# Kernel optimization log

Hardware: AMD Instinct MI355X
Metric: run time of the kernel (lower is better)

Reference implementation:

```python
import jax, jax.numpy as jnp
import numpy as np

N = 50000
E = 600000
IN_DIM, FEAT_DIM, HID_DIM, OUT_DIM = 256, 128, 128, 64


def _glorot(key, shape):
    fan_in, fan_out = shape[0], shape[1]
    lim = jnp.sqrt(6.0 / (fan_in + fan_out))
    return jax.random.uniform(key, shape, jnp.float32, -lim, lim)


def setup_inputs() -> dict:
    key = jax.random.key(0)
    ks = jax.random.split(key, 10)
    x = jax.random.normal(ks[0], (N, IN_DIM), jnp.float32)
    edge_index = jax.random.randint(ks[1], (2, E), 0, N, jnp.int64)
    return {
        "x": x,
        "edge_index": edge_index,
        # linear_pre: input_dim -> feature_dim
        "W_pre": _glorot(ks[2], (IN_DIM, FEAT_DIM)),
        "b_pre": jnp.zeros((FEAT_DIM,), jnp.float32),
        # conv_first (SAGEConv feature_dim -> hidden_dim): lin_l (neighbors, bias), lin_r (root, no bias)
        "Wl1": _glorot(ks[3], (FEAT_DIM, HID_DIM)),
        "bl1": jnp.zeros((HID_DIM,), jnp.float32),
        "Wr1": _glorot(ks[4], (FEAT_DIM, HID_DIM)),
        # conv_out (SAGEConv hidden_dim -> output_dim)
        "Wl2": _glorot(ks[5], (HID_DIM, OUT_DIM)),
        "bl2": jnp.zeros((OUT_DIM,), jnp.float32),
        "Wr2": _glorot(ks[6], (HID_DIM, OUT_DIM)),
    }


def _sage_conv(x, src, dst, deg_inv, Wl, bl, Wr):
    # mean aggregation of source features at destination nodes
    msgs = x[src]                                            # [E, d]
    aggr = jax.ops.segment_sum(msgs, dst, num_segments=N)    # [N, d]
    aggr = aggr * deg_inv[:, None]
    return aggr @ Wl + bl + x @ Wr


def reference(x, edge_index, W_pre, b_pre, Wl1, bl1, Wr1, Wl2, bl2, Wr2):
    src, dst = edge_index[0], edge_index[1]
    deg = jax.ops.segment_sum(jnp.ones((E,), jnp.float32), dst, num_segments=N)
    deg_inv = jnp.where(deg > 0, 1.0 / jnp.maximum(deg, 1.0), 0.0)

    h = x @ W_pre + b_pre                                    # linear_pre
    h = _sage_conv(h, src, dst, deg_inv, Wl1, bl1, Wr1)      # conv_first
    h = jax.nn.relu(h)
    # dropout: identity in eval mode
    h = _sage_conv(h, src, dst, deg_inv, Wl2, bl2, Wr2)      # conv_out
    norm = jnp.linalg.norm(h, axis=-1, keepdims=True)
    return h / jnp.maximum(norm, 1e-12)                      # F.normalize p=2
```

## Files before the change

### kernel.cpp

```cpp
#include <hip/hip_runtime.h>


#define NN   50000
#define EE   600000
#define NBLK 49
#define NRG  1563
#define GEMM_BLOCKS 512

typedef __attribute__((ext_vector_type(8))) _Float16 h8v;
typedef __attribute__((ext_vector_type(4))) _Float16 h4v;
typedef __attribute__((ext_vector_type(2))) _Float16 h2v;
typedef __attribute__((ext_vector_type(8))) short short8v;
typedef __attribute__((ext_vector_type(4))) float f32x4;

__device__ inline h8v h8zero() {
    return __builtin_bit_cast(h8v, (short8v){0,0,0,0,0,0,0,0});
}


__global__ __launch_bounds__(256) void k_count(const int* __restrict__ ei,
                                               int* __restrict__ counts) {
    int e = blockIdx.x * 256 + threadIdx.x;
    if (e < EE) atomicAdd(&counts[ei[EE + e]], 1);
}

__global__ __launch_bounds__(256) void k_scan_a(const int* __restrict__ counts,
                                                int* __restrict__ bsums) {
    int b = blockIdx.x, t = threadIdx.x;
    int idx = b * 1024 + t * 4;
    int s = 0;
#pragma unroll
    for (int j = 0; j < 4; ++j)
        if (idx + j < NN) s += counts[idx + j];
#pragma unroll
    for (int off = 32; off > 0; off >>= 1) s += __shfl_down(s, off);
    __shared__ int ls[4];
    if ((t & 63) == 0) ls[t >> 6] = s;
    __syncthreads();
    if (t == 0) bsums[b] = ls[0] + ls[1] + ls[2] + ls[3];
}

__global__ void k_scan_b(int* __restrict__ bsums) {
    int t = threadIdx.x;
    int v = (t < NBLK) ? bsums[t] : 0;
    int orig = v;
#pragma unroll
    for (int off = 1; off < 64; off <<= 1) {
        int u = __shfl_up(v, off);
        if (t >= off) v += u;
    }
    if (t < NBLK) bsums[t] = v - orig;
}

__global__ __launch_bounds__(256) void k_scan_c(const int* __restrict__ counts,
                                                const int* __restrict__ bsums,
                                                int* __restrict__ rowp) {
    int b = blockIdx.x, t = threadIdx.x;
    int lane = t & 63, wave = t >> 6;
    int idx = b * 1024 + t * 4;
    int c[4], s = 0;
#pragma unroll
    for (int j = 0; j < 4; ++j) {
        c[j] = (idx + j < NN) ? counts[idx + j] : 0;
        s += c[j];
    }
    int sv = s;
#pragma unroll
    for (int off = 1; off < 64; off <<= 1) {
        int u = __shfl_up(sv, off);
        if (lane >= off) sv += u;
    }
    __shared__ int lsum[4];
    if (lane == 63) lsum[wave] = sv;
    __syncthreads();
    int woff = 0;
    for (int wv = 0; wv < wave; ++wv) woff += lsum[wv];
    int base = bsums[b] + woff + (sv - s);
#pragma unroll
    for (int j = 0; j < 4; ++j) {
        if (idx + j < NN) { rowp[idx + j] = base; base += c[j]; }
    }
}

__global__ __launch_bounds__(256) void k_scatter(const int* __restrict__ ei,
                                                 const int* __restrict__ rowp,
                                                 int* __restrict__ cursor,
                                                 int* __restrict__ col) {
    int e = blockIdx.x * 256 + threadIdx.x;
    if (e < EE) {
        int d = ei[EE + e];
        int p = atomicAdd(&cursor[d], 1);
        col[rowp[d] + p] = ei[e];
    }
}


__global__ __launch_bounds__(256) void k_cvt(const float* __restrict__ in,
                                             _Float16* __restrict__ outp, int n4) {
    int i = blockIdx.x * 256 + threadIdx.x;
    if (i >= n4) return;
    float4 v = ((const float4*)in)[i];
    h4v o;
    o[0] = (_Float16)v.x; o[1] = (_Float16)v.y;
    o[2] = (_Float16)v.z; o[3] = (_Float16)v.w;
    ((h4v*)outp)[i] = o;
}


__global__ __launch_bounds__(256) void k_pack(const float* __restrict__ W,
                                              _Float16* __restrict__ hi,
                                              _Float16* __restrict__ lo,
                                              int K, int M) {
    int idx = blockIdx.x * 256 + threadIdx.x;
    if (idx >= K * M) return;
    int k = idx / M, m = idx - k * M;
    float w = W[idx];
    _Float16 h = (_Float16)w;
    hi[m * K + k] = h;
    lo[m * K + k] = (_Float16)(w - (float)h);
}


__global__ __launch_bounds__(256, 2) void k_gemm_pre(
        const _Float16* __restrict__ xh,
        const _Float16* __restrict__ WH, const _Float16* __restrict__ WL,
        const float* __restrict__ bp, _Float16* __restrict__ h0) {
    const int wave = threadIdx.x >> 6, lane = threadIdx.x & 63;
    const int r = lane & 15, kb = lane >> 4;
    const int gw = blockIdx.x * 4 + wave;
    const int col0 = (gw & 3) << 5;

    h8v bh[2][8], bl[2][8];
#pragma unroll
    for (int nt = 0; nt < 2; ++nt)
#pragma unroll
        for (int k = 0; k < 8; ++k) {
            size_t off = (size_t)(col0 + nt * 16 + r) * 256 + k * 32 + kb * 8;
            bh[nt][k] = *(const h8v*)&WH[off];
            bl[nt][k] = *(const h8v*)&WL[off];
        }
    float bias[2];
#pragma unroll
    for (int nt = 0; nt < 2; ++nt) bias[nt] = bp[col0 + nt * 16 + r];

    for (int rg = gw >> 2; rg < NRG; rg += GEMM_BLOCKS) {
        const int row0 = rg << 5;
        f32x4 acc[2][2];
#pragma unroll
        for (int a = 0; a < 2; ++a)
#pragma unroll
            for (int b = 0; b < 2; ++b) acc[a][b] = (f32x4){0.f, 0.f, 0.f, 0.f};

#pragma unroll
        for (int k = 0; k < 8; ++k) {
            h8v ah[2];
#pragma unroll
            for (int rt = 0; rt < 2; ++rt) {
                int rr = row0 + rt * 16;
                ah[rt] = (rr < NN) ? *(const h8v*)&xh[(size_t)(rr + r) * 256 + k * 32 + kb * 8]
                                   : h8zero();
            }
#pragma unroll
            for (int rt = 0; rt < 2; ++rt)
#pragma unroll
                for (int nt = 0; nt < 2; ++nt) {
                    acc[rt][nt] = __builtin_amdgcn_mfma_f32_16x16x32_f16(ah[rt], bh[nt][k], acc[rt][nt], 0, 0, 0);
                    acc[rt][nt] = __builtin_amdgcn_mfma_f32_16x16x32_f16(ah[rt], bl[nt][k], acc[rt][nt], 0, 0, 0);
                }
        }
#pragma unroll
        for (int rt = 0; rt < 2; ++rt) {
            if (row0 + rt * 16 >= NN) continue;
            int rbase = row0 + rt * 16 + kb * 4;
#pragma unroll
            for (int nt = 0; nt < 2; ++nt) {
                int c = col0 + nt * 16 + r;
#pragma unroll
                for (int j = 0; j < 4; ++j)
                    h0[(size_t)(rbase + j) * 128 + c] = (_Float16)(acc[rt][nt][j] + bias[nt]);
            }
        }
    }
}


template <int M>
__global__ __launch_bounds__(256, 2) void k_gemm_dual(
        const _Float16* __restrict__ A,
        const _Float16* __restrict__ W1H, const _Float16* __restrict__ W1L,
        const _Float16* __restrict__ W2H, const _Float16* __restrict__ W2L,
        _Float16* __restrict__ T, _Float16* __restrict__ R) {
    constexpr int CS = M / 32;
    const int wave = threadIdx.x >> 6, lane = threadIdx.x & 63;
    const int r = lane & 15, kb = lane >> 4;
    const int gw = blockIdx.x * 4 + wave;
    const int col0 = (gw % CS) << 5;

    h8v b1h[2][4], b1l[2][4], b2h[2][4], b2l[2][4];
#pragma unroll
    for (int nt = 0; nt < 2; ++nt)
#pragma unroll
        for (int k = 0; k < 4; ++k) {
            size_t off = (size_t)(col0 + nt * 16 + r) * 128 + k * 32 + kb * 8;
            b1h[nt][k] = *(const h8v*)&W1H[off];
            b1l[nt][k] = *(const h8v*)&W1L[off];
            b2h[nt][k] = *(const h8v*)&W2H[off];
            b2l[nt][k] = *(const h8v*)&W2L[off];
        }

    const int stride = (GEMM_BLOCKS * 4) / CS;
    for (int rg = gw / CS; rg < NRG; rg += stride) {
        const int row0 = rg << 5;
        f32x4 accT[2][2], accR[2][2];
#pragma unroll
        for (int a = 0; a < 2; ++a)
#pragma unroll
            for (int b = 0; b < 2; ++b) {
                accT[a][b] = (f32x4){0.f, 0.f, 0.f, 0.f};
                accR[a][b] = (f32x4){0.f, 0.f, 0.f, 0.f};
            }
#pragma unroll
        for (int k = 0; k < 4; ++k) {
            h8v ah[2];
#pragma unroll
            for (int rt = 0; rt < 2; ++rt) {
                int rr = row0 + rt * 16;
                ah[rt] = (rr < NN) ? *(const h8v*)&A[(size_t)(rr + r) * 128 + k * 32 + kb * 8]
                                   : h8zero();
            }
#pragma unroll
            for (int rt = 0; rt < 2; ++rt)
#pragma unroll
                for (int nt = 0; nt < 2; ++nt) {
                    accT[rt][nt] = __builtin_amdgcn_mfma_f32_16x16x32_f16(ah[rt], b1h[nt][k], accT[rt][nt], 0, 0, 0);
                    accT[rt][nt] = __builtin_amdgcn_mfma_f32_16x16x32_f16(ah[rt], b1l[nt][k], accT[rt][nt], 0, 0, 0);
                    accR[rt][nt] = __builtin_amdgcn_mfma_f32_16x16x32_f16(ah[rt], b2h[nt][k], accR[rt][nt], 0, 0, 0);
                    accR[rt][nt] = __builtin_amdgcn_mfma_f32_16x16x32_f16(ah[rt], b2l[nt][k], accR[rt][nt], 0, 0, 0);
                }
        }
#pragma unroll
        for (int rt = 0; rt < 2; ++rt) {
            if (row0 + rt * 16 >= NN) continue;
            int rbase = row0 + rt * 16 + kb * 4;
#pragma unroll
            for (int nt = 0; nt < 2; ++nt) {
                int c = col0 + nt * 16 + r;
#pragma unroll
                for (int j = 0; j < 4; ++j) {
                    T[(size_t)(rbase + j) * M + c] = (_Float16)accT[rt][nt][j];
                    R[(size_t)(rbase + j) * M + c] = (_Float16)accR[rt][nt][j];
                }
            }
        }
    }
}


__global__ __launch_bounds__(256) void k_aggr1(const _Float16* __restrict__ t1,
                                               const _Float16* __restrict__ r1,
                                               const int* __restrict__ rowp,
                                               const int* __restrict__ counts,
                                               const int* __restrict__ col,
                                               const float* __restrict__ bl1,
                                               _Float16* __restrict__ h1) {
    int node = blockIdx.x * 4 + (threadIdx.x >> 6);
    int lane = threadIdx.x & 63;
    if (node >= NN) return;
    int e0 = rowp[node], cnt = counts[node];
    float ax = 0.f, ay = 0.f;
    const h2v* T = (const h2v*)t1;
    for (int base = 0; base < cnt; base += 64) {
        int m = cnt - base; if (m > 64) m = 64;
        int myS = (base + lane < cnt) ? col[e0 + base + lane] : 0;
        int i = 0;
        for (; i + 8 <= m; i += 8) {
            int s0 = __shfl(myS, i + 0), s1 = __shfl(myS, i + 1);
            int s2 = __shfl(myS, i + 2), s3 = __shfl(myS, i + 3);
            int s4 = __shfl(myS, i + 4), s5 = __shfl(myS, i + 5);
            int s6 = __shfl(myS, i + 6), s7 = __shfl(myS, i + 7);
            h2v v0 = T[(size_t)s0 * 64 + lane], v1 = T[(size_t)s1 * 64 + lane];
            h2v v2 = T[(size_t)s2 * 64 + lane], v3 = T[(size_t)s3 * 64 + lane];
            h2v v4 = T[(size_t)s4 * 64 + lane], v5 = T[(size_t)s5 * 64 + lane];
            h2v v6 = T[(size_t)s6 * 64 + lane], v7 = T[(size_t)s7 * 64 + lane];
            ax += (float)v0[0] + (float)v1[0] + (float)v2[0] + (float)v3[0]
                + (float)v4[0] + (float)v5[0] + (float)v6[0] + (float)v7[0];
            ay += (float)v0[1] + (float)v1[1] + (float)v2[1] + (float)v3[1]
                + (float)v4[1] + (float)v5[1] + (float)v6[1] + (float)v7[1];
        }
        for (; i < m; ++i) {
            int s = __shfl(myS, i);
            h2v v = T[(size_t)s * 64 + lane];
            ax += (float)v[0]; ay += (float)v[1];
        }
    }
    float di = (cnt > 0) ? 1.0f / (float)cnt : 0.0f;
    h2v rr = ((const h2v*)r1)[(size_t)node * 64 + lane];
    float2 bb = ((const float2*)bl1)[lane];
    float hx = fmaxf(fmaf(ax, di, bb.x + (float)rr[0]), 0.0f);
    float hy = fmaxf(fmaf(ay, di, bb.y + (float)rr[1]), 0.0f);
    h2v h; h[0] = (_Float16)hx; h[1] = (_Float16)hy;
    ((h2v*)h1)[(size_t)node * 64 + lane] = h;
}


__global__ __launch_bounds__(256) void k_aggr2(const _Float16* __restrict__ t2,
                                               const _Float16* __restrict__ r2,
                                               const int* __restrict__ rowp,
                                               const int* __restrict__ counts,
                                               const int* __restrict__ col,
                                               const float* __restrict__ bl2,
                                               float* __restrict__ out) {
    int node = blockIdx.x * 4 + (threadIdx.x >> 6);
    int lane = threadIdx.x & 63;
    if (node >= NN) return;
    int half = lane >> 5, sl = lane & 31;
    int e0 = rowp[node], cnt = counts[node];
    float ax = 0.f, ay = 0.f;
    const h2v* T = (const h2v*)t2;
    for (int base = 0; base < cnt; base += 64) {
        int m = cnt - base; if (m > 64) m = 64;
        int myS = (base + lane < cnt) ? col[e0 + base + lane] : 0;
        int i = 0;
        for (; i + 8 <= m; i += 8) {
            int s0 = __shfl(myS, i + 0 + half), s1 = __shfl(myS, i + 2 + half);
            int s2 = __shfl(myS, i + 4 + half), s3 = __shfl(myS, i + 6 + half);
            h2v v0 = T[(size_t)s0 * 32 + sl], v1 = T[(size_t)s1 * 32 + sl];
            h2v v2 = T[(size_t)s2 * 32 + sl], v3 = T[(size_t)s3 * 32 + sl];
            ax += (float)v0[0] + (float)v1[0] + (float)v2[0] + (float)v3[0];
            ay += (float)v0[1] + (float)v1[1] + (float)v2[1] + (float)v3[1];
        }
        for (; i < m; i += 2) {
            if (i + half < m) {
                int s = __shfl(myS, i + half);
                h2v v = T[(size_t)s * 32 + sl];
                ax += (float)v[0]; ay += (float)v[1];
            }
        }
    }
    ax += __shfl_xor(ax, 32);
    ay += __shfl_xor(ay, 32);
    float di = (cnt > 0) ? 1.0f / (float)cnt : 0.0f;
    h2v rr = ((const h2v*)r2)[(size_t)node * 32 + sl];
    float2 bb = ((const float2*)bl2)[sl];
    float v0 = fmaf(ax, di, bb.x + (float)rr[0]);
    float v1 = fmaf(ay, di, bb.y + (float)rr[1]);
    float ss = v0 * v0 + v1 * v1;
#pragma unroll
    for (int off = 16; off > 0; off >>= 1) ss += __shfl_xor(ss, off);
    float inv = 1.0f / fmaxf(sqrtf(ss), 1e-12f);
    if (half == 0)
        ((float2*)out)[(size_t)node * 32 + sl] = make_float2(v0 * inv, v1 * inv);
}


extern "C" void kernel_launch(void* const* d_in, const int* in_sizes, int n_in,
                              void* d_out, int out_size, void* d_ws, size_t ws_size,
                              hipStream_t stream) {
    const float* x    = (const float*)d_in[0];
    const int*   ei   = (const int*)d_in[1];
    const float* Wpre = (const float*)d_in[2];
    const float* bpre = (const float*)d_in[3];
    const float* Wl1  = (const float*)d_in[4];
    const float* bl1  = (const float*)d_in[5];
    const float* Wr1  = (const float*)d_in[6];
    const float* Wl2  = (const float*)d_in[7];
    const float* bl2  = (const float*)d_in[8];
    const float* Wr2  = (const float*)d_in[9];
    float* out = (float*)d_out;

    char* w = (char*)d_ws;
    int* counts = (int*)w;  w += (size_t)NN * 4;
    int* cursor = (int*)w;  w += (size_t)NN * 4;
    int* rowp   = (int*)w;  w += (size_t)NN * 4;
    int* bsums  = (int*)w;  w += 256;
    int* col    = (int*)w;  w += (size_t)EE * 4;
    _Float16* WpH  = (_Float16*)w; w += (size_t)256 * 128 * 2;
    _Float16* WpL  = (_Float16*)w; w += (size_t)256 * 128 * 2;
    _Float16* W1lH = (_Float16*)w; w += (size_t)128 * 128 * 2;
    _Float16* W1lL = (_Float16*)w; w += (size_t)128 * 128 * 2;
    _Float16* W1rH = (_Float16*)w; w += (size_t)128 * 128 * 2;
    _Float16* W1rL = (_Float16*)w; w += (size_t)128 * 128 * 2;
    _Float16* W2lH = (_Float16*)w; w += (size_t)128 * 64 * 2;
    _Float16* W2lL = (_Float16*)w; w += (size_t)128 * 64 * 2;
    _Float16* W2rH = (_Float16*)w; w += (size_t)128 * 64 * 2;
    _Float16* W2rL = (_Float16*)w; w += (size_t)128 * 64 * 2;
    _Float16* xh   = (_Float16*)w; w += (size_t)NN * 256 * 2;
    _Float16* h0   = (_Float16*)w; w += (size_t)NN * 128 * 2;
    _Float16* t1   = (_Float16*)w; w += (size_t)NN * 128 * 2;
    _Float16* r1   = (_Float16*)w; w += (size_t)NN * 128 * 2;
    _Float16* h1   = (_Float16*)w; w += (size_t)NN * 128 * 2;
    _Float16* t2   = (_Float16*)w; w += (size_t)NN * 64 * 2;
    _Float16* r2   = (_Float16*)w; w += (size_t)NN * 64 * 2;

    hipMemsetAsync(counts, 0, (size_t)NN * 8, stream);

    dim3 b256(256);
    dim3 gE((EE + 255) / 256);
    k_count<<<gE, b256, 0, stream>>>(ei, counts);
    k_scan_a<<<dim3(NBLK), b256, 0, stream>>>(counts, bsums);
    k_scan_b<<<dim3(1), dim3(64), 0, stream>>>(bsums);
    k_scan_c<<<dim3(NBLK), b256, 0, stream>>>(counts, bsums, rowp);
    k_scatter<<<gE, b256, 0, stream>>>(ei, rowp, cursor, col);

    k_cvt<<<dim3(NN * 256 / 4 / 256), b256, 0, stream>>>(x, xh, NN * 256 / 4);
    k_pack<<<dim3(128), b256, 0, stream>>>(Wpre, WpH, WpL, 256, 128);
    k_pack<<<dim3(64),  b256, 0, stream>>>(Wl1, W1lH, W1lL, 128, 128);
    k_pack<<<dim3(64),  b256, 0, stream>>>(Wr1, W1rH, W1rL, 128, 128);
    k_pack<<<dim3(32),  b256, 0, stream>>>(Wl2, W2lH, W2lL, 128, 64);
    k_pack<<<dim3(32),  b256, 0, stream>>>(Wr2, W2rH, W2rL, 128, 64);

    dim3 gP(GEMM_BLOCKS);
    k_gemm_pre<<<gP, b256, 0, stream>>>(xh, WpH, WpL, bpre, h0);
    k_gemm_dual<128><<<gP, b256, 0, stream>>>(h0, W1lH, W1lL, W1rH, W1rL, t1, r1);
    k_aggr1<<<dim3((NN + 3) / 4), b256, 0, stream>>>(t1, r1, rowp, counts, col, bl1, h1);
    k_gemm_dual<64><<<gP, b256, 0, stream>>>(h1, W2lH, W2lL, W2rH, W2rL, t2, r2);
    k_aggr2<<<dim3((NN + 3) / 4), b256, 0, stream>>>(t2, r2, rowp, counts, col, bl2, out);
}
```

Before: 304.5 us.

## Fold linear_pre into first SAGE weights and fuse input conversion into GEMM

Since there is no nonlinearity between linear_pre and conv_first, the weights are pre-multiplied (Wpre·Wl1, Wpre·Wr1, bias folded) in a small kernel. A single GEMM then reads fp32 x directly, converts it in registers and produces t1/r1. This removes the x→fp16 conversion pass, the h0 intermediate and one GEMM. The K dimension of the remaining GEMM grows from 128 to 256, and the pre-multiplied weights are rounded to fp16 hi/lo differently, so numerics shift slightly. Separately, aggr1 now gathers 4 halves per lane, with the two half-waves handling alternating edges and a final cross-half reduction.

```diff
diff --git a/kernel.cpp b/kernel.cpp
--- a/kernel.cpp
+++ b/kernel.cpp
@@ -15,6 +15,17 @@
 
 __device__ inline h8v h8zero() {
     return __builtin_bit_cast(h8v, (short8v){0,0,0,0,0,0,0,0});
+}
+
+__device__ inline h8v cvt8(const float* __restrict__ p) {
+    float4 f0 = *(const float4*)p;
+    float4 f1 = *(const float4*)(p + 4);
+    h8v a;
+    a[0] = (_Float16)f0.x; a[1] = (_Float16)f0.y;
+    a[2] = (_Float16)f0.z; a[3] = (_Float16)f0.w;
+    a[4] = (_Float16)f1.x; a[5] = (_Float16)f1.y;
+    a[6] = (_Float16)f1.z; a[7] = (_Float16)f1.w;
+    return a;
 }
 
 
@@ -95,89 +106,107 @@
 }
 
 
-__global__ __launch_bounds__(256) void k_cvt(const float* __restrict__ in,
-                                             _Float16* __restrict__ outp, int n4) {
-    int i = blockIdx.x * 256 + threadIdx.x;
-    if (i >= n4) return;
-    float4 v = ((const float4*)in)[i];
-    h4v o;
-    o[0] = (_Float16)v.x; o[1] = (_Float16)v.y;
-    o[2] = (_Float16)v.z; o[3] = (_Float16)v.w;
-    ((h4v*)outp)[i] = o;
-}
-
-
-__global__ __launch_bounds__(256) void k_pack(const float* __restrict__ W,
-                                              _Float16* __restrict__ hi,
-                                              _Float16* __restrict__ lo,
-                                              int K, int M) {
+__global__ __launch_bounds__(256) void k_fuse(const float* __restrict__ Wpre,
+                                              const float* __restrict__ bpre,
+                                              const float* __restrict__ Wl1,
+                                              const float* __restrict__ Wr1,
+                                              _Float16* __restrict__ WAH,
+                                              _Float16* __restrict__ WAL,
+                                              _Float16* __restrict__ WBH,
+                                              _Float16* __restrict__ WBL,
+                                              float* __restrict__ bA,
+                                              float* __restrict__ bB) {
     int idx = blockIdx.x * 256 + threadIdx.x;
-    if (idx >= K * M) return;
-    int k = idx / M, m = idx - k * M;
-    float w = W[idx];
+    int which = idx / (257 * 128);
+    int rem = idx - which * 257 * 128;
+    int i = rem >> 7, j = rem & 127;
+    const float* W = which ? Wr1 : Wl1;
+    float s = 0.f;
+    if (i < 256) {
+#pragma unroll 4
+        for (int k = 0; k < 128; ++k) s += Wpre[i * 128 + k] * W[k * 128 + j];
+        _Float16 h = (_Float16)s;
+        _Float16 l = (_Float16)(s - (float)h);
+        if (which) { WBH[j * 256 + i] = h; WBL[j * 256 + i] = l; }
+        else       { WAH[j * 256 + i] = h; WAL[j * 256 + i] = l; }
+    } else {
+#pragma unroll 4
+        for (int k = 0; k < 128; ++k) s += bpre[k] * W[k * 128 + j];
+        if (which) bB[j] = s; else bA[j] = s;
+    }
+}
+
+
+__global__ __launch_bounds__(256) void k_pack2(const float* __restrict__ Wl2,
+                                               const float* __restrict__ Wr2,
+                                               _Float16* __restrict__ W2lH,
+                                               _Float16* __restrict__ W2lL,
+                                               _Float16* __restrict__ W2rH,
+                                               _Float16* __restrict__ W2rL) {
+    int idx = blockIdx.x * 256 + threadIdx.x;
+    int which = idx >> 13;
+    int rem = idx & 8191;
+    int k = rem >> 6, m = rem & 63;
+    float w = (which ? Wr2 : Wl2)[rem];
     _Float16 h = (_Float16)w;
-    hi[m * K + k] = h;
-    lo[m * K + k] = (_Float16)(w - (float)h);
-}
-
-
-__global__ __launch_bounds__(256, 2) void k_gemm_pre(
-        const _Float16* __restrict__ xh,
-        const _Float16* __restrict__ WH, const _Float16* __restrict__ WL,
-        const float* __restrict__ bp, _Float16* __restrict__ h0) {
+    _Float16 l = (_Float16)(w - (float)h);
+    if (which) { W2rH[m * 128 + k] = h; W2rL[m * 128 + k] = l; }
+    else       { W2lH[m * 128 + k] = h; W2lL[m * 128 + k] = l; }
+}
+
+
+__global__ __launch_bounds__(256, 2) void k_gemm_fused(
+        const float* __restrict__ x,
+        const _Float16* __restrict__ WAH, const _Float16* __restrict__ WAL,
+        const _Float16* __restrict__ WBH, const _Float16* __restrict__ WBL,
+        const float* __restrict__ bA, const float* __restrict__ bB,
+        _Float16* __restrict__ t1, _Float16* __restrict__ r1) {
     const int wave = threadIdx.x >> 6, lane = threadIdx.x & 63;
     const int r = lane & 15, kb = lane >> 4;
     const int gw = blockIdx.x * 4 + wave;
-    const int col0 = (gw & 3) << 5;
-
-    h8v bh[2][8], bl[2][8];
-#pragma unroll
-    for (int nt = 0; nt < 2; ++nt)
+    const int col = ((gw & 7) << 4) + r;
+
+    h8v wah[8], wal[8], wbh[8], wbl[8];
+#pragma unroll
+    for (int k = 0; k < 8; ++k) {
+        size_t off = (size_t)col * 256 + k * 32 + kb * 8;
+        wah[k] = *(const h8v*)&WAH[off];
+        wal[k] = *(const h8v*)&WAL[off];
+        wbh[k] = *(const h8v*)&WBH[off];
+        wbl[k] = *(const h8v*)&WBL[off];
+    }
+    const float biasA = bA[col], biasB = bB[col];
+
+    for (int rg = gw >> 3; rg < NRG; rg += (GEMM_BLOCKS * 4) / 8) {
+        const int row0 = rg << 5;
+        f32x4 accT[2], accR[2];
+#pragma unroll
+        for (int a = 0; a < 2; ++a) {
+            accT[a] = (f32x4){0.f, 0.f, 0.f, 0.f};
+            accR[a] = (f32x4){0.f, 0.f, 0.f, 0.f};
+        }
 #pragma unroll
         for (int k = 0; k < 8; ++k) {
-            size_t off = (size_t)(col0 + nt * 16 + r) * 256 + k * 32 + kb * 8;
-            bh[nt][k] = *(const h8v*)&WH[off];
-            bl[nt][k] = *(const h8v*)&WL[off];
-        }
-    float bias[2];
-#pragma unroll
-    for (int nt = 0; nt < 2; ++nt) bias[nt] = bp[col0 + nt * 16 + r];
-
-    for (int rg = gw >> 2; rg < NRG; rg += GEMM_BLOCKS) {
-        const int row0 = rg << 5;
-        f32x4 acc[2][2];
-#pragma unroll
-        for (int a = 0; a < 2; ++a)
-#pragma unroll
-            for (int b = 0; b < 2; ++b) acc[a][b] = (f32x4){0.f, 0.f, 0.f, 0.f};
-
-#pragma unroll
-        for (int k = 0; k < 8; ++k) {
-            h8v ah[2];
 #pragma unroll
             for (int rt = 0; rt < 2; ++rt) {
                 int rr = row0 + rt * 16;
-                ah[rt] = (rr < NN) ? *(const h8v*)&xh[(size_t)(rr + r) * 256 + k * 32 + kb * 8]
-                                   : h8zero();
-            }
-#pragma unroll
-            for (int rt = 0; rt < 2; ++rt)
-#pragma unroll
-                for (int nt = 0; nt < 2; ++nt) {
-                    acc[rt][nt] = __builtin_amdgcn_mfma_f32_16x16x32_f16(ah[rt], bh[nt][k], acc[rt][nt], 0, 0, 0);
-                    acc[rt][nt] = __builtin_amdgcn_mfma_f32_16x16x32_f16(ah[rt], bl[nt][k], acc[rt][nt], 0, 0, 0);
-                }
+                h8v a = (rr < NN)
+                    ? cvt8(&x[(size_t)(rr + r) * 256 + k * 32 + kb * 8])
+                    : h8zero();
+                accT[rt] = __builtin_amdgcn_mfma_f32_16x16x32_f16(a, wah[k], accT[rt], 0, 0, 0);
+                accT[rt] = __builtin_amdgcn_mfma_f32_16x16x32_f16(a, wal[k], accT[rt], 0, 0, 0);
+                accR[rt] = __builtin_amdgcn_mfma_f32_16x16x32_f16(a, wbh[k], accR[rt], 0, 0, 0);
+                accR[rt] = __builtin_amdgcn_mfma_f32_16x16x32_f16(a, wbl[k], accR[rt], 0, 0, 0);
+            }
         }
 #pragma unroll
         for (int rt = 0; rt < 2; ++rt) {
             if (row0 + rt * 16 >= NN) continue;
             int rbase = row0 + rt * 16 + kb * 4;
 #pragma unroll
-            for (int nt = 0; nt < 2; ++nt) {
-                int c = col0 + nt * 16 + r;
-#pragma unroll
-                for (int j = 0; j < 4; ++j)
-                    h0[(size_t)(rbase + j) * 128 + c] = (_Float16)(acc[rt][nt][j] + bias[nt]);
+            for (int j = 0; j < 4; ++j) {
+                t1[(size_t)(rbase + j) * 128 + col] = (_Float16)(accT[rt][j] + biasA);
+                r1[(size_t)(rbase + j) * 128 + col] = (_Float16)(accR[rt][j] + biasB);
             }
         }
     }
@@ -266,40 +295,46 @@
     int node = blockIdx.x * 4 + (threadIdx.x >> 6);
     int lane = threadIdx.x & 63;
     if (node >= NN) return;
+    int half = lane >> 5, sl = lane & 31;
     int e0 = rowp[node], cnt = counts[node];
-    float ax = 0.f, ay = 0.f;
-    const h2v* T = (const h2v*)t1;
+    float a0 = 0.f, a1 = 0.f, a2 = 0.f, a3 = 0.f;
+    const h4v* T = (const h4v*)t1;
     for (int base = 0; base < cnt; base += 64) {
         int m = cnt - base; if (m > 64) m = 64;
         int myS = (base + lane < cnt) ? col[e0 + base + lane] : 0;
         int i = 0;
         for (; i + 8 <= m; i += 8) {
-            int s0 = __shfl(myS, i + 0), s1 = __shfl(myS, i + 1);
-            int s2 = __shfl(myS, i + 2), s3 = __shfl(myS, i + 3);
-            int s4 = __shfl(myS, i + 4), s5 = __shfl(myS, i + 5);
-            int s6 = __shfl(myS, i + 6), s7 = __shfl(myS, i + 7);
-            h2v v0 = T[(size_t)s0 * 64 + lane], v1 = T[(size_t)s1 * 64 + lane];
-            h2v v2 = T[(size_t)s2 * 64 + lane], v3 = T[(size_t)s3 * 64 + lane];
-            h2v v4 = T[(size_t)s4 * 64 + lane], v5 = T[(size_t)s5 * 64 + lane];
-            h2v v6 = T[(size_t)s6 * 64 + lane], v7 = T[(size_t)s7 * 64 + lane];
-            ax += (float)v0[0] + (float)v1[0] + (float)v2[0] + (float)v3[0]
-                + (float)v4[0] + (float)v5[0] + (float)v6[0] + (float)v7[0];
-            ay += (float)v0[1] + (float)v1[1] + (float)v2[1] + (float)v3[1]
-                + (float)v4[1] + (float)v5[1] + (float)v6[1] + (float)v7[1];
-        }
-        for (; i < m; ++i) {
-            int s = __shfl(myS, i);
-            h2v v = T[(size_t)s * 64 + lane];
-            ax += (float)v[0]; ay += (float)v[1];
-        }
-    }
+            int s0 = __shfl(myS, i + 0 + half), s1 = __shfl(myS, i + 2 + half);
+            int s2 = __shfl(myS, i + 4 + half), s3 = __shfl(myS, i + 6 + half);
+            h4v v0 = T[(size_t)s0 * 32 + sl], v1 = T[(size_t)s1 * 32 + sl];
+            h4v v2 = T[(size_t)s2 * 32 + sl], v3 = T[(size_t)s3 * 32 + sl];
+            a0 += (float)v0[0] + (float)v1[0] + (float)v2[0] + (float)v3[0];
+            a1 += (float)v0[1] + (float)v1[1] + (float)v2[1] + (float)v3[1];
+            a2 += (float)v0[2] + (float)v1[2] + (float)v2[2] + (float)v3[2];
+            a3 += (float)v0[3] + (float)v1[3] + (float)v2[3] + (float)v3[3];
+        }
+        for (; i < m; i += 2) {
+            if (i + half < m) {
+                int s = __shfl(myS, i + half);
+                h4v v = T[(size_t)s * 32 + sl];
+                a0 += (float)v[0]; a1 += (float)v[1];
+                a2 += (float)v[2]; a3 += (float)v[3];
+            }
+        }
+    }
+    a0 += __shfl_xor(a0, 32); a1 += __shfl_xor(a1, 32);
+    a2 += __shfl_xor(a2, 32); a3 += __shfl_xor(a3, 32);
     float di = (cnt > 0) ? 1.0f / (float)cnt : 0.0f;
-    h2v rr = ((const h2v*)r1)[(size_t)node * 64 + lane];
-    float2 bb = ((const float2*)bl1)[lane];
-    float hx = fmaxf(fmaf(ax, di, bb.x + (float)rr[0]), 0.0f);
-    float hy = fmaxf(fmaf(ay, di, bb.y + (float)rr[1]), 0.0f);
-    h2v h; h[0] = (_Float16)hx; h[1] = (_Float16)hy;
-    ((h2v*)h1)[(size_t)node * 64 + lane] = h;
+    h4v rr = ((const h4v*)r1)[(size_t)node * 32 + sl];
+    float4 bb = ((const float4*)bl1)[sl];
+    if (half == 0) {
+        h4v h;
+        h[0] = (_Float16)fmaxf(fmaf(a0, di, bb.x + (float)rr[0]), 0.0f);
+        h[1] = (_Float16)fmaxf(fmaf(a1, di, bb.y + (float)rr[1]), 0.0f);
+        h[2] = (_Float16)fmaxf(fmaf(a2, di, bb.z + (float)rr[2]), 0.0f);
+        h[3] = (_Float16)fmaxf(fmaf(a3, di, bb.w + (float)rr[3]), 0.0f);
+        ((h4v*)h1)[(size_t)node * 32 + sl] = h;
+    }
 }
 
 
@@ -374,18 +409,16 @@
     int* rowp   = (int*)w;  w += (size_t)NN * 4;
     int* bsums  = (int*)w;  w += 256;
     int* col    = (int*)w;  w += (size_t)EE * 4;
-    _Float16* WpH  = (_Float16*)w; w += (size_t)256 * 128 * 2;
-    _Float16* WpL  = (_Float16*)w; w += (size_t)256 * 128 * 2;
-    _Float16* W1lH = (_Float16*)w; w += (size_t)128 * 128 * 2;
-    _Float16* W1lL = (_Float16*)w; w += (size_t)128 * 128 * 2;
-    _Float16* W1rH = (_Float16*)w; w += (size_t)128 * 128 * 2;
-    _Float16* W1rL = (_Float16*)w; w += (size_t)128 * 128 * 2;
+    _Float16* WAH  = (_Float16*)w; w += (size_t)256 * 128 * 2;
+    _Float16* WAL  = (_Float16*)w; w += (size_t)256 * 128 * 2;
+    _Float16* WBH  = (_Float16*)w; w += (size_t)256 * 128 * 2;
+    _Float16* WBL  = (_Float16*)w; w += (size_t)256 * 128 * 2;
+    float*    bA   = (float*)w;    w += 128 * 4;
+    float*    bB   = (float*)w;    w += 128 * 4;
     _Float16* W2lH = (_Float16*)w; w += (size_t)128 * 64 * 2;
     _Float16* W2lL = (_Float16*)w; w += (size_t)128 * 64 * 2;
     _Float16* W2rH = (_Float16*)w; w += (size_t)128 * 64 * 2;
     _Float16* W2rL = (_Float16*)w; w += (size_t)128 * 64 * 2;
-    _Float16* xh   = (_Float16*)w; w += (size_t)NN * 256 * 2;
-    _Float16* h0   = (_Float16*)w; w += (size_t)NN * 128 * 2;
     _Float16* t1   = (_Float16*)w; w += (size_t)NN * 128 * 2;
     _Float16* r1   = (_Float16*)w; w += (size_t)NN * 128 * 2;
     _Float16* h1   = (_Float16*)w; w += (size_t)NN * 128 * 2;
@@ -402,16 +435,12 @@
     k_scan_c<<<dim3(NBLK), b256, 0, stream>>>(counts, bsums, rowp);
     k_scatter<<<gE, b256, 0, stream>>>(ei, rowp, cursor, col);
 
-    k_cvt<<<dim3(NN * 256 / 4 / 256), b256, 0, stream>>>(x, xh, NN * 256 / 4);
-    k_pack<<<dim3(128), b256, 0, stream>>>(Wpre, WpH, WpL, 256, 128);
-    k_pack<<<dim3(64),  b256, 0, stream>>>(Wl1, W1lH, W1lL, 128, 128);
-    k_pack<<<dim3(64),  b256, 0, stream>>>(Wr1, W1rH, W1rL, 128, 128);
-    k_pack<<<dim3(32),  b256, 0, stream>>>(Wl2, W2lH, W2lL, 128, 64);
-    k_pack<<<dim3(32),  b256, 0, stream>>>(Wr2, W2rH, W2rL, 128, 64);
+    k_fuse<<<dim3(257), b256, 0, stream>>>(Wpre, bpre, Wl1, Wr1,
+                                           WAH, WAL, WBH, WBL, bA, bB);
+    k_pack2<<<dim3(64), b256, 0, stream>>>(Wl2, Wr2, W2lH, W2lL, W2rH, W2rL);
 
     dim3 gP(GEMM_BLOCKS);
-    k_gemm_pre<<<gP, b256, 0, stream>>>(xh, WpH, WpL, bpre, h0);
-    k_gemm_dual<128><<<gP, b256, 0, stream>>>(h0, W1lH, W1lL, W1rH, W1rL, t1, r1);
+    k_gemm_fused<<<gP, b256, 0, stream>>>(x, WAH, WAL, WBH, WBL, bA, bB, t1, r1);
     k_aggr1<<<dim3((NN + 3) / 4), b256, 0, stream>>>(t1, r1, rowp, counts, col, bl1, h1);
     k_gemm_dual<64><<<gP, b256, 0, stream>>>(h1, W2lH, W2lL, W2rH, W2rL, t2, r2);
     k_aggr2<<<dim3((NN + 3) / 4), b256, 0, stream>>>(t2, r2, rowp, counts, col, bl2, out);
```

Result: slower. 322.2 us (+5.8%).
